# Performance work log

Measured on AMD Instinct MI355X. Metric: run time of the kernel, lower is better.

Reference implementation:

```python
import jax, jax.numpy as jnp
import numpy as np

K = 512   # cardinality of each hidden source
O = 8     # n_out per party
NS = 3    # number of sources (triangle network)


def setup_inputs() -> dict:
    key = jax.random.key(0)
    k1, k2 = jax.random.split(key)
    n_pred = NS * K + 3 * K * K * O
    y_pred = jax.random.uniform(k1, (1, n_pred), dtype=jnp.float32)
    y_true = jax.random.uniform(k2, (O ** 3,), dtype=jnp.float32)
    y_true = y_true / jnp.sum(y_true)  # a proper target distribution
    return {"y_pred": y_pred, "y_true": y_true}


def _distribution(y_pred):
    # sources block: [NS, K] source probability tables
    srcs = y_pred[0, :NS * K].reshape(NS, K)
    pf = y_pred[0, NS * K:]
    sz = K * K * O
    # party response tensors, indexed by the two source symbols the party sees
    A = pf[:sz].reshape(K, K, O)          # A sees (beta, gamma) -> (j, k)
    B = pf[sz:2 * sz].reshape(K, K, O)    # B sees (gamma, alpha) -> (k, i)
    C = pf[2 * sz:].reshape(K, K, O)      # C sees (alpha, beta) -> (i, j)
    Pa, Pb, Pc = srcs[0], srcs[1], srcs[2]
    # prob[x,y,z] = sum_{i,j,k} Pa[i] Pb[j] Pc[k] A[j,k,x] B[k,i,y] C[i,j,z]
    Aw = A * Pb[:, None, None] * Pc[None, :, None]   # [j,k,x]
    Bw = B * Pa[None, :, None]                        # [k,i,y]
    T = jnp.einsum('jkx,kiy->ijxy', Aw, Bw)           # contract k; [K,K,O,O]
    probs = jnp.einsum('ijxy,ijz->xyz', T, C)         # contract i,j; [O,O,O]
    return probs.reshape(-1)


def reference(y_pred, y_true):
    probs = _distribution(y_pred)
    log_p = jnp.log(jnp.clip(probs, 1e-10, 1.0))
    d = jnp.sum(y_true * (jnp.log(y_true + 1e-10) - log_p))
    return (d, probs)
```

## Files before the change

### kernel.cpp

```cpp
#include <hip/hip_runtime.h>
#include <hip/hip_bf16.h>
#include <stdint.h>

#define KD 512
#define OD 8
#define SZ (KD*KD*OD)
#define PLANE (KD*KD)

typedef short v8s __attribute__((ext_vector_type(8)));
typedef float v4f __attribute__((ext_vector_type(4)));

#define GLOBAL_AS __attribute__((address_space(1)))
#define LDS_AS __attribute__((address_space(3)))

static __device__ __forceinline__ unsigned short f2bf(float f) {
    union { float f; unsigned int u; } v; v.f = f;
    unsigned int u = v.u;
    unsigned int r = u + 0x7FFF + ((u >> 16) & 1);
    return (unsigned short)(r >> 16);
}

static __device__ __forceinline__ void async16(const unsigned short* g, unsigned short* l) {
    __builtin_amdgcn_global_load_lds((const GLOBAL_AS void*)g, (LDS_AS void*)l, 16, 0, 0);
}

static __device__ __forceinline__ void bar() {
    __builtin_amdgcn_sched_barrier(0);
    __builtin_amdgcn_s_barrier();
    __builtin_amdgcn_sched_barrier(0);
}


__global__ __launch_bounds__(256) void pack_kernel(const float* __restrict__ yp,
                                                   unsigned short* __restrict__ Wbf,
                                                   unsigned short* __restrict__ Xbf,
                                                   float* __restrict__ probs_acc) {
    __shared__ unsigned short lds[8192];
    const float* Pa = yp;
    const float* Pb = yp + KD;
    const float* Pc = yp + 2 * KD;
    const float* A  = yp + 3 * KD;
    const float* B  = A + SZ;
    const int b = blockIdx.x;
    const int t = threadIdx.x;

    if (b == 0) { probs_acc[t] = 0.0f; probs_acc[t + 256] = 0.0f; }

    if (b < 256) {
        const int jt = b >> 3, kb = b & 7;
        const int j0 = jt * 16, k0 = kb * 64;
        #pragma unroll
        for (int cc = 0; cc < 2; ++cc) {
            const int cell = cc * 256 + t;
            const int kl = (cell & 31) * 2;
            const int jl = cell >> 5;
            const int j = j0 + jl, k = k0 + kl;
            const float pb = Pb[j];
            const float s0 = pb * Pc[k];
            const float s1 = pb * Pc[k + 1];
            const float4* src = (const float4*)(A + ((size_t)j * KD + k) * 8);
            float av[16];
            ((float4*)av)[0] = src[0];
            ((float4*)av)[1] = src[1];
            ((float4*)av)[2] = src[2];
            ((float4*)av)[3] = src[3];
            const int swz = (jl & 7) << 3;
            #pragma unroll
            for (int x = 0; x < 8; ++x) {
                ushort2 wv;
                wv.x = f2bf(av[x] * s0);
                wv.y = f2bf(av[8 + x] * s1);
                *(ushort2*)&lds[jl * 512 + x * 64 + (kl ^ swz)] = wv;
            }
        }
        __syncthreads();
        #pragma unroll
        for (int ss = 0; ss < 4; ++ss) {
            const int slot = ss * 256 + t;
            const int x = slot >> 7;
            const int kcc = (slot >> 6) & 1;
            const int l = slot & 63;
            const int jl = l & 15, kq = l >> 4;
            const int klocal = kcc * 32 + kq * 8;
            const int swz = (jl & 7) << 3;
            uint4 v = *(const uint4*)&lds[jl * 512 + x * 64 + (klocal ^ swz)];
            const size_t fo = (size_t)(kb * 2 + kcc) * 16384 + (size_t)jt * 512 + l * 8;
            *(uint4*)(Wbf + (size_t)x * PLANE + fo) = v;
        }
    } else {
        const int tb = b - 256;
        const int k0 = (tb / 16) * 32;
        const int i0 = (tb % 16) * 32;
        char* ldsb = (char*)lds;
        #pragma unroll
        for (int p = 0; p < 4; ++p) {
            const int idx = t + p * 256;
            const int dk = idx >> 5;
            const int di = idx & 31;
            const float pa = Pa[i0 + di];
            const float4* src = (const float4*)(B + ((size_t)(k0 + dk) * KD + (i0 + di)) * 8);
            float bv[8];
            ((float4*)bv)[0] = src[0];
            ((float4*)bv)[1] = src[1];
            const int swz = (di & 7) << 4;
            #pragma unroll
            for (int y = 0; y < 8; ++y)
                *(unsigned short*)(ldsb + (y * 32 + di) * 64 + ((dk * 2) ^ swz)) =
                    f2bf(bv[y] * pa);
        }
        __syncthreads();
        #pragma unroll
        for (int p = 0; p < 4; ++p) {
            const int c = t + p * 256;
            const int y = c >> 7;
            const int rem = c & 127;
            const int di = rem >> 2;
            const int dk8 = (rem & 3) * 8;
            uint4 v = *(const uint4*)(ldsb + (y * 32 + di) * 64 + ((dk8 * 2) ^ ((di & 7) << 4)));
            const size_t fo = (size_t)(k0 >> 5) * 16384 + (size_t)((i0 + di) >> 4) * 512
                            + (size_t)(dk8 >> 3) * 128 + (di & 15) * 8;
            *(uint4*)(Xbf + (size_t)y * PLANE + fo) = v;
        }
    }
}

__global__ __launch_bounds__(512, 2) void gemm_kernel(const float* __restrict__ yp,
                                                      const unsigned short* __restrict__ Wbf,
                                                      const unsigned short* __restrict__ Xbf,
                                                      float* __restrict__ probs_acc) {
    __shared__ unsigned short S[2][32 * 512];
    __shared__ float red[8][32];

    const int bid = blockIdx.x;
    const int xcd = bid & 7;
    const int local = bid >> 3;
    const int tl = local >> 4;
    const int group = local & 15;
    const int i_t = xcd >> 1;
    const int j_t = ((xcd & 1) << 1) | tl;
    const int i0 = i_t * 128, j0 = j_t * 128;
    const int x0 = (group >> 2) * 2, y0 = (group & 3) * 2;

    const int t = threadIdx.x;
    const int w = t >> 6;
    const int l = t & 63;
    const int wm = w >> 2, wn = w & 3;
    const int lm = l & 15, quad = l >> 4;

    const unsigned short* gq[4];
    #pragma unroll
    for (int q = 0; q < 4; ++q) {
        const int idx = w * 4 + q;
        const int tile = idx >> 3;
        const int rt = idx & 7;
        if (tile < 2)
            gq[q] = Xbf + (size_t)(y0 + tile) * PLANE + (size_t)(i0 / 16 + rt) * 512 + l * 8;
        else
            gq[q] = Wbf + (size_t)(x0 + (tile - 2)) * PLANE + (size_t)(j0 / 16 + rt) * 512 + l * 8;
    }
    const int sbase = (w * 4) * 512;

    v4f acc[2][2][4][2];
    #pragma unroll
    for (int a = 0; a < 2; ++a)
      #pragma unroll
      for (int bb = 0; bb < 2; ++bb)
        #pragma unroll
        for (int c = 0; c < 4; ++c)
          #pragma unroll
          for (int d = 0; d < 2; ++d)
            acc[a][bb][c][d] = (v4f){0.f, 0.f, 0.f, 0.f};

    #pragma unroll
    for (int q = 0; q < 4; ++q) async16(gq[q], &S[0][sbase + q * 512]);
    #pragma unroll
    for (int q = 0; q < 4; ++q) async16(gq[q] + 16384, &S[1][sbase + q * 512]);
    asm volatile("s_waitcnt vmcnt(4)" ::: "memory");
    bar();

    for (int kc = 0; kc < 16; ++kc) {
        const int cur = kc & 1;
        v8s aF[2][4], bF[2][2];
        #pragma unroll
        for (int dy = 0; dy < 2; ++dy)
            #pragma unroll
            for (int mt = 0; mt < 4; ++mt)
                aF[dy][mt] = *(const v8s*)&S[cur][(dy * 8 + wm * 4 + mt) * 512 + l * 8];
        #pragma unroll
        for (int dx = 0; dx < 2; ++dx)
            #pragma unroll
            for (int nt = 0; nt < 2; ++nt)
                bF[dx][nt] = *(const v8s*)&S[cur][((2 + dx) * 8 + wn * 2 + nt) * 512 + l * 8];
        __builtin_amdgcn_s_setprio(1);
        #pragma unroll
        for (int dy = 0; dy < 2; ++dy)
            #pragma unroll
            for (int dx = 0; dx < 2; ++dx)
                #pragma unroll
                for (int mt = 0; mt < 4; ++mt)
                    #pragma unroll
                    for (int nt = 0; nt < 2; ++nt)
                        acc[dy][dx][mt][nt] = __builtin_amdgcn_mfma_f32_16x16x32_bf16(
                            aF[dy][mt], bF[dx][nt], acc[dy][dx][mt][nt], 0, 0, 0);
        __builtin_amdgcn_s_setprio(0);
        bar();
        if (kc + 2 < 16) {
            const size_t kb = (size_t)(kc + 2) * 16384;
            #pragma unroll
            for (int q = 0; q < 4; ++q) async16(gq[q] + kb, &S[cur][sbase + q * 512]);
        }
        if (kc < 15) {
            if (kc + 2 < 16) asm volatile("s_waitcnt vmcnt(4)" ::: "memory");
            else             asm volatile("s_waitcnt vmcnt(0)" ::: "memory");
            bar();
        }
    }

    const float* Cp = yp + 3 * KD + 2 * (size_t)SZ;
    float zacc[2][2][8];
    #pragma unroll
    for (int dy = 0; dy < 2; ++dy)
      #pragma unroll
      for (int dx = 0; dx < 2; ++dx)
        #pragma unroll
        for (int z = 0; z < 8; ++z) zacc[dy][dx][z] = 0.f;

    #pragma unroll
    for (int mt = 0; mt < 4; ++mt) {
        #pragma unroll
        for (int nt = 0; nt < 2; ++nt) {
            #pragma unroll
            for (int r = 0; r < 4; ++r) {
                const int gi = i0 + wm * 64 + mt * 16 + quad * 4 + r;
                const int gj = j0 + wn * 32 + nt * 16 + lm;
                const float4* cp = (const float4*)(Cp + ((size_t)gi * KD + gj) * 8);
                const float4 c0 = cp[0], c1 = cp[1];
                #pragma unroll
                for (int dy = 0; dy < 2; ++dy) {
                    #pragma unroll
                    for (int dx = 0; dx < 2; ++dx) {
                        const float tv = acc[dy][dx][mt][nt][r];
                        zacc[dy][dx][0] += tv * c0.x; zacc[dy][dx][1] += tv * c0.y;
                        zacc[dy][dx][2] += tv * c0.z; zacc[dy][dx][3] += tv * c0.w;
                        zacc[dy][dx][4] += tv * c1.x; zacc[dy][dx][5] += tv * c1.y;
                        zacc[dy][dx][6] += tv * c1.z; zacc[dy][dx][7] += tv * c1.w;
                    }
                }
            }
        }
    }
    #pragma unroll
    for (int dy = 0; dy < 2; ++dy)
      #pragma unroll
      for (int dx = 0; dx < 2; ++dx)
        #pragma unroll
        for (int z = 0; z < 8; ++z) {
            float v = zacc[dy][dx][z];
            for (int off = 32; off > 0; off >>= 1)
                v += __shfl_xor(v, off, 64);
            zacc[dy][dx][z] = v;
        }
    if (l == 0) {
        #pragma unroll
        for (int dy = 0; dy < 2; ++dy)
          #pragma unroll
          for (int dx = 0; dx < 2; ++dx)
            #pragma unroll
            for (int z = 0; z < 8; ++z)
                red[w][(dy * 2 + dx) * 8 + z] = zacc[dy][dx][z];
    }
    __syncthreads();
    if (t < 32) {
        float s = 0.f;
        #pragma unroll
        for (int ww = 0; ww < 8; ++ww) s += red[ww][t];
        const int p = t >> 3;
        const int dy = p >> 1, dx = p & 1, z = t & 7;
        atomicAdd(&probs_acc[((x0 + dx) * 8 + (y0 + dy)) * 8 + z], s);
    }
}

__global__ __launch_bounds__(512) void finalize_kernel(const float* __restrict__ probs_acc,
                                                       const float* __restrict__ y_true,
                                                       float* __restrict__ out) {
    __shared__ float red[8];
    const int t = threadIdx.x;
    const float p = probs_acc[t];
    out[1 + t] = p;
    const float ytv = y_true[t];
    const float pc = fminf(fmaxf(p, 1e-10f), 1.0f);
    float term = ytv * (logf(ytv + 1e-10f) - logf(pc));
    for (int off = 32; off > 0; off >>= 1)
        term += __shfl_xor(term, off, 64);
    if ((t & 63) == 0) red[t >> 6] = term;
    __syncthreads();
    if (t == 0) {
        float s = 0.f;
        #pragma unroll
        for (int i = 0; i < 8; ++i) s += red[i];
        out[0] = s;
    }
}

extern "C" void kernel_launch(void* const* d_in, const int* in_sizes, int n_in,
                              void* d_out, int out_size, void* d_ws, size_t ws_size,
                              hipStream_t stream) {
    const float* yp = (const float*)d_in[0];
    const float* yt = (const float*)d_in[1];
    float* out = (float*)d_out;

    unsigned short* Wbf = (unsigned short*)d_ws;
    unsigned short* Xbf = Wbf + (size_t)8 * PLANE;
    float* probs_acc = (float*)(Xbf + (size_t)8 * PLANE);

    pack_kernel<<<512, 256, 0, stream>>>(yp, Wbf, Xbf, probs_acc);
    gemm_kernel<<<256, 512, 0, stream>>>(yp, Wbf, Xbf, probs_acc);
    finalize_kernel<<<1, 512, 0, stream>>>(probs_acc, yt, out);
}
```

Baseline: 100.2 us.

## Fuse pack, GEMM and finalize into one persistent kernel with grid barriers

Merges the bf16 pack stage, the MFMA GEMM and the KL finalize into a single 256-block kernel. An atomic counter acts as a grid-wide barrier between packing and GEMM, and a second counter lets block 0 run the finalize once every block has finished. A tiny init kernel zeroes the accumulator and counters. This removes two kernel launches and their gaps, but the whole grid must be co-resident for the spin barrier, and each block now does the work of two former pack blocks.

```diff
diff --git a/kernel.cpp b/kernel.cpp
--- a/kernel.cpp
+++ b/kernel.cpp
@@ -30,30 +30,40 @@
     __builtin_amdgcn_sched_barrier(0);
 }
 
-
-__global__ __launch_bounds__(256) void pack_kernel(const float* __restrict__ yp,
-                                                   unsigned short* __restrict__ Wbf,
-                                                   unsigned short* __restrict__ Xbf,
-                                                   float* __restrict__ probs_acc) {
-    __shared__ unsigned short lds[8192];
+__global__ __launch_bounds__(512) void init_kernel(float* __restrict__ probs_acc,
+                                                   unsigned* __restrict__ ctr) {
+    const int t = threadIdx.x;
+    probs_acc[t] = 0.0f;
+    if (t < 2) ctr[t] = 0u;
+}
+
+__global__ __launch_bounds__(512, 2) void fused_kernel(const float* __restrict__ yp,
+                                                       unsigned short* __restrict__ Wbf,
+                                                       unsigned short* __restrict__ Xbf,
+                                                       float* __restrict__ probs_acc,
+                                                       unsigned* __restrict__ ctr,
+                                                       const float* __restrict__ y_true,
+                                                       float* __restrict__ out) {
+    __shared__ unsigned short S[2][32 * 512];
+    __shared__ float red[8][32];
+
+    const int bid = blockIdx.x;
+    const int t = threadIdx.x;
+
     const float* Pa = yp;
     const float* Pb = yp + KD;
     const float* Pc = yp + 2 * KD;
     const float* A  = yp + 3 * KD;
     const float* B  = A + SZ;
-    const int b = blockIdx.x;
-    const int t = threadIdx.x;
-
-    if (b == 0) { probs_acc[t] = 0.0f; probs_acc[t + 256] = 0.0f; }
-
-    if (b < 256) {
-        const int jt = b >> 3, kb = b & 7;
+
+    unsigned short* lds = &S[0][0];
+
+    {
+        const int jt = bid >> 3, kb = bid & 7;
         const int j0 = jt * 16, k0 = kb * 64;
-        #pragma unroll
-        for (int cc = 0; cc < 2; ++cc) {
-            const int cell = cc * 256 + t;
-            const int kl = (cell & 31) * 2;
-            const int jl = cell >> 5;
+        {
+            const int kl = (t & 31) * 2;
+            const int jl = t >> 5;
             const int j = j0 + jl, k = k0 + kl;
             const float pb = Pb[j];
             const float s0 = pb * Pc[k];
@@ -74,31 +84,32 @@
             }
         }
         __syncthreads();
-        #pragma unroll
-        for (int ss = 0; ss < 4; ++ss) {
-            const int slot = ss * 256 + t;
-            const int x = slot >> 7;
-            const int kcc = (slot >> 6) & 1;
-            const int l = slot & 63;
-            const int jl = l & 15, kq = l >> 4;
-            const int klocal = kcc * 32 + kq * 8;
-            const int swz = (jl & 7) << 3;
-            uint4 v = *(const uint4*)&lds[jl * 512 + x * 64 + (klocal ^ swz)];
-            const size_t fo = (size_t)(kb * 2 + kcc) * 16384 + (size_t)jt * 512 + l * 8;
-            *(uint4*)(Wbf + (size_t)x * PLANE + fo) = v;
-        }
-    } else {
-        const int tb = b - 256;
-        const int k0 = (tb / 16) * 32;
-        const int i0 = (tb % 16) * 32;
+        {
+            #pragma unroll
+            for (int ss = 0; ss < 2; ++ss) {
+                const int slot = ss * 512 + t;
+                const int x = slot >> 7;
+                const int kcc = (slot >> 6) & 1;
+                const int l = slot & 63;
+                const int jl = l & 15, kq = l >> 4;
+                const int klocal = kcc * 32 + kq * 8;
+                const int swz = (jl & 7) << 3;
+                uint4 v = *(const uint4*)&lds[jl * 512 + x * 64 + (klocal ^ swz)];
+                const size_t fo = (size_t)(kb * 2 + kcc) * 16384 + (size_t)jt * 512 + l * 8;
+                *(uint4*)(Wbf + (size_t)x * PLANE + fo) = v;
+            }
+        }
+        __syncthreads();
+        const int k0b = (bid / 16) * 32;
+        const int i0b = (bid % 16) * 32;
         char* ldsb = (char*)lds;
         #pragma unroll
-        for (int p = 0; p < 4; ++p) {
-            const int idx = t + p * 256;
+        for (int p = 0; p < 2; ++p) {
+            const int idx = t + p * 512;
             const int dk = idx >> 5;
             const int di = idx & 31;
-            const float pa = Pa[i0 + di];
-            const float4* src = (const float4*)(B + ((size_t)(k0 + dk) * KD + (i0 + di)) * 8);
+            const float pa = Pa[i0b + di];
+            const float4* src = (const float4*)(B + ((size_t)(k0b + dk) * KD + (i0b + di)) * 8);
             float bv[8];
             ((float4*)bv)[0] = src[0];
             ((float4*)bv)[1] = src[1];
@@ -110,28 +121,29 @@
         }
         __syncthreads();
         #pragma unroll
-        for (int p = 0; p < 4; ++p) {
-            const int c = t + p * 256;
+        for (int p = 0; p < 2; ++p) {
+            const int c = t + p * 512;
             const int y = c >> 7;
             const int rem = c & 127;
             const int di = rem >> 2;
             const int dk8 = (rem & 3) * 8;
             uint4 v = *(const uint4*)(ldsb + (y * 32 + di) * 64 + ((dk8 * 2) ^ ((di & 7) << 4)));
-            const size_t fo = (size_t)(k0 >> 5) * 16384 + (size_t)((i0 + di) >> 4) * 512
+            const size_t fo = (size_t)(k0b >> 5) * 16384 + (size_t)((i0b + di) >> 4) * 512
                             + (size_t)(dk8 >> 3) * 128 + (di & 15) * 8;
             *(uint4*)(Xbf + (size_t)y * PLANE + fo) = v;
         }
     }
-}
-
-__global__ __launch_bounds__(512, 2) void gemm_kernel(const float* __restrict__ yp,
-                                                      const unsigned short* __restrict__ Wbf,
-                                                      const unsigned short* __restrict__ Xbf,
-                                                      float* __restrict__ probs_acc) {
-    __shared__ unsigned short S[2][32 * 512];
-    __shared__ float red[8][32];
-
-    const int bid = blockIdx.x;
+
+    __syncthreads();
+    if (t == 0) {
+        __threadfence();
+        __hip_atomic_fetch_add(&ctr[0], 1u, __ATOMIC_RELEASE, __HIP_MEMORY_SCOPE_AGENT);
+        while (__hip_atomic_load(&ctr[0], __ATOMIC_ACQUIRE, __HIP_MEMORY_SCOPE_AGENT) < 256u)
+            __builtin_amdgcn_s_sleep(2);
+        __threadfence();
+    }
+    __syncthreads();
+
     const int xcd = bid & 7;
     const int local = bid >> 3;
     const int tl = local >> 4;
@@ -141,7 +153,6 @@
     const int i0 = i_t * 128, j0 = j_t * 128;
     const int x0 = (group >> 2) * 2, y0 = (group & 3) * 2;
 
-    const int t = threadIdx.x;
     const int w = t >> 6;
     const int l = t & 63;
     const int wm = w >> 2, wn = w & 3;
@@ -205,9 +216,9 @@
         __builtin_amdgcn_s_setprio(0);
         bar();
         if (kc + 2 < 16) {
-            const size_t kb = (size_t)(kc + 2) * 16384;
-            #pragma unroll
-            for (int q = 0; q < 4; ++q) async16(gq[q] + kb, &S[cur][sbase + q * 512]);
+            const size_t kb2 = (size_t)(kc + 2) * 16384;
+            #pragma unroll
+            for (int q = 0; q < 4; ++q) async16(gq[q] + kb2, &S[cur][sbase + q * 512]);
         }
         if (kc < 15) {
             if (kc + 2 < 16) asm volatile("s_waitcnt vmcnt(4)" ::: "memory");
@@ -278,27 +289,37 @@
         const int dy = p >> 1, dx = p & 1, z = t & 7;
         atomicAdd(&probs_acc[((x0 + dx) * 8 + (y0 + dy)) * 8 + z], s);
     }
-}
-
-__global__ __launch_bounds__(512) void finalize_kernel(const float* __restrict__ probs_acc,
-                                                       const float* __restrict__ y_true,
-                                                       float* __restrict__ out) {
-    __shared__ float red[8];
-    const int t = threadIdx.x;
-    const float p = probs_acc[t];
-    out[1 + t] = p;
-    const float ytv = y_true[t];
-    const float pc = fminf(fmaxf(p, 1e-10f), 1.0f);
-    float term = ytv * (logf(ytv + 1e-10f) - logf(pc));
-    for (int off = 32; off > 0; off >>= 1)
-        term += __shfl_xor(term, off, 64);
-    if ((t & 63) == 0) red[t >> 6] = term;
-    __syncthreads();
+
+    __syncthreads();
+    if (bid != 0) {
+        if (t == 0)
+            __hip_atomic_fetch_add(&ctr[1], 1u, __ATOMIC_RELEASE, __HIP_MEMORY_SCOPE_AGENT);
+        return;
+    }
     if (t == 0) {
-        float s = 0.f;
-        #pragma unroll
-        for (int i = 0; i < 8; ++i) s += red[i];
-        out[0] = s;
+        __hip_atomic_fetch_add(&ctr[1], 1u, __ATOMIC_RELEASE, __HIP_MEMORY_SCOPE_AGENT);
+        while (__hip_atomic_load(&ctr[1], __ATOMIC_ACQUIRE, __HIP_MEMORY_SCOPE_AGENT) < 256u)
+            __builtin_amdgcn_s_sleep(2);
+    }
+    __syncthreads();
+
+    {
+        const float p = __hip_atomic_load(&probs_acc[t], __ATOMIC_RELAXED,
+                                          __HIP_MEMORY_SCOPE_AGENT);
+        out[1 + t] = p;
+        const float ytv = y_true[t];
+        const float pc = fminf(fmaxf(p, 1e-10f), 1.0f);
+        float term = ytv * (logf(ytv + 1e-10f) - logf(pc));
+        for (int off = 32; off > 0; off >>= 1)
+            term += __shfl_xor(term, off, 64);
+        if (l == 0) red[w][0] = term;
+        __syncthreads();
+        if (t == 0) {
+            float s = 0.f;
+            #pragma unroll
+            for (int i = 0; i < 8; ++i) s += red[i][0];
+            out[0] = s;
+        }
     }
 }
 
@@ -312,8 +333,8 @@
     unsigned short* Wbf = (unsigned short*)d_ws;
     unsigned short* Xbf = Wbf + (size_t)8 * PLANE;
     float* probs_acc = (float*)(Xbf + (size_t)8 * PLANE);
-
-    pack_kernel<<<512, 256, 0, stream>>>(yp, Wbf, Xbf, probs_acc);
-    gemm_kernel<<<256, 512, 0, stream>>>(yp, Wbf, Xbf, probs_acc);
-    finalize_kernel<<<1, 512, 0, stream>>>(probs_acc, yt, out);
-}
+    unsigned* ctr = (unsigned*)(probs_acc + 512);
+
+    init_kernel<<<1, 512, 0, stream>>>(probs_acc, ctr);
+    fused_kernel<<<256, 512, 0, stream>>>(yp, Wbf, Xbf, probs_acc, ctr, yt, out);
+}
```

Result: slower. 130.9 us (+30.6%).
